# Optimization experiments

Measured on AMD Instinct MI355X. Metric: run time of the kernel, lower is better.

Reference implementation:

```python
import jax, jax.numpy as jnp
import numpy as np

# Structural constants (mirror init_kwargs)
P = 64    # n_poses
R = 128   # rotamers per pose
A = 8     # atoms per rotamer
EPS = 1e-2  # distance clamp to avoid singularity


def setup_inputs() -> dict:
    key = jax.random.key(0)
    n_rots = P * R
    coords = jax.random.normal(key, (n_rots * A, 3), dtype=jnp.float32) * 3.0
    coord_offset_for_rot = (jnp.arange(n_rots, dtype=jnp.int32) * A)
    pose_for_rot = jnp.repeat(jnp.arange(P, dtype=jnp.int32), R)
    rot_offset_for_pose = jnp.arange(P, dtype=jnp.int32) * R
    return {
        "coords": coords,
        "coord_offset_for_rot": coord_offset_for_rot,
        "pose_for_rot": pose_for_rot,
        "rot_offset_for_pose": rot_offset_for_pose,
    }


def reference(coords, coord_offset_for_rot, pose_for_rot, rot_offset_for_pose):
    # flatten leading dims to [n_atoms_total, 3] (matches coords.flatten(0,-2))
    flat = coords.reshape(-1, 3)
    # gather each rotamer's atoms via its coordinate offset: [n_rots, A]
    atom_idx = coord_offset_for_rot[:, None] + jnp.arange(A, dtype=jnp.int32)[None, :]
    x = flat[atom_idx]                       # [n_rots, A, 3]
    x = x.reshape(P, R, A, 3)                # block per pose
    # squared pairwise atom distances between all rotamer pairs within a pose
    sq = jnp.sum(x * x, axis=-1)             # [P, R, A]
    dot = jnp.einsum('piac,pjbc->pijab', x, x)   # [P, R, R, A, A]
    d2 = sq[:, :, None, :, None] + sq[:, None, :, None, :] - 2.0 * dot
    d2 = jnp.maximum(d2, EPS)
    # two subterm energies summed over atom pairs -> [P, R, R]
    s0 = jnp.sum(1.0 / d2, axis=(-2, -1))                  # LJ-like repulsion
    s1 = jnp.sum(jnp.exp(-jnp.sqrt(d2)), axis=(-2, -1))    # LK-like decay
    scores = jnp.stack([s0.reshape(-1), s1.reshape(-1)], axis=0)  # [2, nnz]
    # indices [3, nnz]: (pose, global rot_i, global rot_j)
    r = jnp.arange(R, dtype=jnp.int32)
    ii, jj = jnp.meshgrid(r, r, indexing='ij')             # [R, R]
    pose_idx = jnp.repeat(pose_for_rot, R)                 # [P*R*R]
    rot_i = (rot_offset_for_pose[:, None, None] + ii[None]).reshape(-1)
    rot_j = (rot_offset_for_pose[:, None, None] + jj[None]).reshape(-1)
    indices = jnp.stack([pose_idx, rot_i, rot_j], axis=0).astype(jnp.int32)
    return scores, indices
```

## Files before the change

### kernel.cpp

```cpp
#include <hip/hip_runtime.h>

typedef float v2f __attribute__((ext_vector_type(2)));

#define NPOSE 64
#define NROT  128
#define NATOM 8
#define EPS   1e-2f

#define TS    16
#define NTILE (NROT / TS)
#define NPAIR (NTILE * (NTILE + 1) / 2)
#define CSTR  28
#define SSTR  17

__global__ __launch_bounds__(256, 4) void rot_score_kernel(
    const float* __restrict__ coords,
    float* __restrict__ out)
{
    __shared__ float ldsI[TS * CSTR];
    __shared__ float ldsJ[TS * CSTR];
    __shared__ float res0[TS * SSTR];
    __shared__ float res1[TS * SSTR];

    const int bid = blockIdx.x;
    const int p   = bid / NPAIR;
    int t = bid - p * NPAIR;
    int ti = 0;
    while (t >= NTILE - ti) { t -= NTILE - ti; ++ti; }
    const int tj = ti + t;

    const int tid = threadIdx.x;
    const float* src = coords + (size_t)p * (NROT * NATOM * 3);

    for (int idx = tid; idx < 2 * TS * 24; idx += 256) {
        const int set = idx >= TS * 24;
        const int loc = idx - set * (TS * 24);
        const int r   = loc / 24;
        const int k   = loc - r * 24;
        const float v = src[(set ? tj : ti) * (TS * 24) + loc];
        (set ? ldsJ : ldsI)[r * CSTR + k] = v;
    }
    __syncthreads();

    const int ty = tid >> 4;
    const int tx = tid & 15;

    float4 xi4[6], xj4[6];
    {
        const float4* rowI = (const float4*)&ldsI[ty * CSTR];
        const float4* rowJ = (const float4*)&ldsJ[tx * CSTR];
#pragma unroll
        for (int k = 0; k < 6; ++k) { xi4[k] = rowI[k]; xj4[k] = rowJ[k]; }
    }
    float* xi = (float*)xi4;
    const float* xj = (const float*)xj4;

    float sqi[NATOM];
#pragma unroll
    for (int a = 0; a < NATOM; ++a)
        sqi[a] = fmaf(xi[a*3+2], xi[a*3+2], fmaf(xi[a*3+1], xi[a*3+1], xi[a*3+0]*xi[a*3+0]));
#pragma unroll
    for (int k = 0; k < 24; ++k) xi[k] = xi[k] * -2.0f;

    const float SCH_S = -12102203.0f;
    const float SCH_B = 1064866805.0f;
    const v2f veps = { EPS, EPS };

    v2f s0v = { 0.0f, 0.0f }, s1v = { 0.0f, 0.0f };

#pragma unroll
    for (int bp = 0; bp < 4; ++bp) {
        const v2f ax = { xj[bp*6 + 0], xj[bp*6 + 3] };
        const v2f ay = { xj[bp*6 + 1], xj[bp*6 + 4] };
        const v2f az = { xj[bp*6 + 2], xj[bp*6 + 5] };
        const v2f sj = __builtin_elementwise_fma(az, az,
                        __builtin_elementwise_fma(ay, ay, ax * ax));
#pragma unroll
        for (int a = 0; a < NATOM; ++a) {
            v2f t = sj + sqi[a];
            t = __builtin_elementwise_fma((v2f)(xi[a*3+0]), ax, t);
            t = __builtin_elementwise_fma((v2f)(xi[a*3+1]), ay, t);
            t = __builtin_elementwise_fma((v2f)(xi[a*3+2]), az, t);
            t = __builtin_elementwise_max(t, veps);
            const v2f rs = { __builtin_amdgcn_rsqf(t.x),
                             __builtin_amdgcn_rsqf(t.y) };
            s0v = __builtin_elementwise_fma(rs, rs, s0v);
            const v2f dv = t * rs;
            const v2f st = __builtin_elementwise_fma(dv, (v2f)(SCH_S), (v2f)(SCH_B));
            v2f e;
            e.x = __int_as_float((int)st.x);
            e.y = __int_as_float((int)st.y);
            s1v += e;
        }
    }
    const float s0 = s0v.x + s0v.y;
    const float s1 = s1v.x + s1v.y;

    res0[ty * SSTR + tx] = s0;
    res1[ty * SSTR + tx] = s1;

    const int nnz = NPOSE * NROT * NROT;
    const int gi  = ti * TS + ty;
    const int gj  = tj * TS + tx;
    const int n   = (p * NROT + gi) * NROT + gj;

    out[0 * nnz + n] = s0;
    out[1 * nnz + n] = s1;
    out[2 * nnz + n] = (float)p;
    out[3 * nnz + n] = (float)(p * NROT + gi);
    out[4 * nnz + n] = (float)(p * NROT + gj);

    if (ti != tj) {
        __syncthreads();
        const float m0 = res0[tx * SSTR + ty];
        const float m1 = res1[tx * SSTR + ty];
        const int mi = tj * TS + ty;
        const int mj = ti * TS + tx;
        const int nm = (p * NROT + mi) * NROT + mj;
        out[0 * nnz + nm] = m0;
        out[1 * nnz + nm] = m1;
        out[2 * nnz + nm] = (float)p;
        out[3 * nnz + nm] = (float)(p * NROT + mi);
        out[4 * nnz + nm] = (float)(p * NROT + mj);
    }
}

extern "C" void kernel_launch(void* const* d_in, const int* in_sizes, int n_in,
                              void* d_out, int out_size, void* d_ws, size_t ws_size,
                              hipStream_t stream) {
    (void)in_sizes; (void)n_in; (void)d_ws; (void)ws_size; (void)out_size;
    const float* coords = (const float*)d_in[0];
    float* out = (float*)d_out;

    dim3 grid(NPOSE * NPAIR);
    dim3 block(256);
    rot_score_kernel<<<grid, block, 0, stream>>>(coords, out);
}
```

Measured before the change: 19.06 us.

## Compute two j-rotamers per thread with 128-thread blocks and float2 stores

Halves the block to 128 threads and has each thread compute two output columns, packing the two j-rotamers into the v2f lanes instead of two atom pairs. The i-rotamer coordinates are reused across both columns, and all output writes become float2 vector stores. This cuts redundant loads of i-coordinates and the number of store instructions, but doubles per-thread work and register pressure and leaves fewer waves per block to hide latency.

```diff
diff --git a/kernel.cpp b/kernel.cpp
--- a/kernel.cpp
+++ b/kernel.cpp
@@ -13,7 +13,7 @@
 #define CSTR  28
 #define SSTR  17
 
-__global__ __launch_bounds__(256, 4) void rot_score_kernel(
+__global__ __launch_bounds__(128, 4) void rot_score_kernel(
     const float* __restrict__ coords,
     float* __restrict__ out)
 {
@@ -32,7 +32,7 @@
     const int tid = threadIdx.x;
     const float* src = coords + (size_t)p * (NROT * NATOM * 3);
 
-    for (int idx = tid; idx < 2 * TS * 24; idx += 256) {
+    for (int idx = tid; idx < 2 * TS * 24; idx += 128) {
         const int set = idx >= TS * 24;
         const int loc = idx - set * (TS * 24);
         const int r   = loc / 24;
@@ -42,18 +42,16 @@
     }
     __syncthreads();
 
-    const int ty = tid >> 4;
-    const int tx = tid & 15;
+    const int ty  = tid >> 3;
+    const int txp = tid & 7;
 
-    float4 xi4[6], xj4[6];
+    float4 xi4[6];
     {
         const float4* rowI = (const float4*)&ldsI[ty * CSTR];
-        const float4* rowJ = (const float4*)&ldsJ[tx * CSTR];
 #pragma unroll
-        for (int k = 0; k < 6; ++k) { xi4[k] = rowI[k]; xj4[k] = rowJ[k]; }
+        for (int k = 0; k < 6; ++k) xi4[k] = rowI[k];
     }
     float* xi = (float*)xi4;
-    const float* xj = (const float*)xj4;
 
     float sqi[NATOM];
 #pragma unroll
@@ -65,63 +63,88 @@
     const float SCH_S = -12102203.0f;
     const float SCH_B = 1064866805.0f;
     const v2f veps = { EPS, EPS };
+    const float* rowJA = &ldsJ[(txp * 2 + 0) * CSTR];
+    const float* rowJB = &ldsJ[(txp * 2 + 1) * CSTR];
 
     v2f s0v = { 0.0f, 0.0f }, s1v = { 0.0f, 0.0f };
 
 #pragma unroll
     for (int bp = 0; bp < 4; ++bp) {
-        const v2f ax = { xj[bp*6 + 0], xj[bp*6 + 3] };
-        const v2f ay = { xj[bp*6 + 1], xj[bp*6 + 4] };
-        const v2f az = { xj[bp*6 + 2], xj[bp*6 + 5] };
-        const v2f sj = __builtin_elementwise_fma(az, az,
-                        __builtin_elementwise_fma(ay, ay, ax * ax));
+        const float A0 = rowJA[bp*6 + 0], A1 = rowJA[bp*6 + 1], A2 = rowJA[bp*6 + 2];
+        const float A3 = rowJA[bp*6 + 3], A4 = rowJA[bp*6 + 4], A5 = rowJA[bp*6 + 5];
+        const float B0 = rowJB[bp*6 + 0], B1 = rowJB[bp*6 + 1], B2 = rowJB[bp*6 + 2];
+        const float B3 = rowJB[bp*6 + 3], B4 = rowJB[bp*6 + 4], B5 = rowJB[bp*6 + 5];
+        const v2f ex = { A0, B0 }, ey = { A1, B1 }, ez = { A2, B2 };
+        const v2f ox = { A3, B3 }, oy = { A4, B4 }, oz = { A5, B5 };
+        const v2f sje = __builtin_elementwise_fma(ez, ez,
+                         __builtin_elementwise_fma(ey, ey, ex * ex));
+        const v2f sjo = __builtin_elementwise_fma(oz, oz,
+                         __builtin_elementwise_fma(oy, oy, ox * ox));
 #pragma unroll
         for (int a = 0; a < NATOM; ++a) {
-            v2f t = sj + sqi[a];
-            t = __builtin_elementwise_fma((v2f)(xi[a*3+0]), ax, t);
-            t = __builtin_elementwise_fma((v2f)(xi[a*3+1]), ay, t);
-            t = __builtin_elementwise_fma((v2f)(xi[a*3+2]), az, t);
-            t = __builtin_elementwise_max(t, veps);
-            const v2f rs = { __builtin_amdgcn_rsqf(t.x),
-                             __builtin_amdgcn_rsqf(t.y) };
-            s0v = __builtin_elementwise_fma(rs, rs, s0v);
-            const v2f dv = t * rs;
-            const v2f st = __builtin_elementwise_fma(dv, (v2f)(SCH_S), (v2f)(SCH_B));
-            v2f e;
-            e.x = __int_as_float((int)st.x);
-            e.y = __int_as_float((int)st.y);
-            s1v += e;
+            v2f te = sje + sqi[a];
+            te = __builtin_elementwise_fma((v2f)(xi[a*3+0]), ex, te);
+            te = __builtin_elementwise_fma((v2f)(xi[a*3+1]), ey, te);
+            te = __builtin_elementwise_fma((v2f)(xi[a*3+2]), ez, te);
+            te = __builtin_elementwise_max(te, veps);
+            const v2f rse = { __builtin_amdgcn_rsqf(te.x), __builtin_amdgcn_rsqf(te.y) };
+            s0v = __builtin_elementwise_fma(rse, rse, s0v);
+            const v2f dve = te * rse;
+            const v2f ste = __builtin_elementwise_fma(dve, (v2f)(SCH_S), (v2f)(SCH_B));
+            v2f ee; ee.x = __int_as_float((int)ste.x); ee.y = __int_as_float((int)ste.y);
+            s1v += ee;
+
+            v2f to = sjo + sqi[a];
+            to = __builtin_elementwise_fma((v2f)(xi[a*3+0]), ox, to);
+            to = __builtin_elementwise_fma((v2f)(xi[a*3+1]), oy, to);
+            to = __builtin_elementwise_fma((v2f)(xi[a*3+2]), oz, to);
+            to = __builtin_elementwise_max(to, veps);
+            const v2f rso = { __builtin_amdgcn_rsqf(to.x), __builtin_amdgcn_rsqf(to.y) };
+            s0v = __builtin_elementwise_fma(rso, rso, s0v);
+            const v2f dvo = to * rso;
+            const v2f sto = __builtin_elementwise_fma(dvo, (v2f)(SCH_S), (v2f)(SCH_B));
+            v2f eo; eo.x = __int_as_float((int)sto.x); eo.y = __int_as_float((int)sto.y);
+            s1v += eo;
         }
     }
-    const float s0 = s0v.x + s0v.y;
-    const float s1 = s1v.x + s1v.y;
 
-    res0[ty * SSTR + tx] = s0;
-    res1[ty * SSTR + tx] = s1;
+    res0[ty * SSTR + txp * 2 + 0] = s0v.x;
+    res0[ty * SSTR + txp * 2 + 1] = s0v.y;
+    res1[ty * SSTR + txp * 2 + 0] = s1v.x;
+    res1[ty * SSTR + txp * 2 + 1] = s1v.y;
 
-    const int nnz = NPOSE * NROT * NROT;
-    const int gi  = ti * TS + ty;
-    const int gj  = tj * TS + tx;
-    const int n   = (p * NROT + gi) * NROT + gj;
+    const int nnz  = NPOSE * NROT * NROT;
+    const int gi   = ti * TS + ty;
+    const int col0 = tj * TS + txp * 2;
+    const int n    = (p * NROT + gi) * NROT + col0;
 
-    out[0 * nnz + n] = s0;
-    out[1 * nnz + n] = s1;
-    out[2 * nnz + n] = (float)p;
-    out[3 * nnz + n] = (float)(p * NROT + gi);
-    out[4 * nnz + n] = (float)(p * NROT + gj);
+    const float fp  = (float)p;
+    const float ri  = (float)(p * NROT + gi);
+    const float rj0 = (float)(p * NROT + col0);
+
+    *(float2*)(out + (size_t)0 * nnz + n) = make_float2(s0v.x, s0v.y);
+    *(float2*)(out + (size_t)1 * nnz + n) = make_float2(s1v.x, s1v.y);
+    *(float2*)(out + (size_t)2 * nnz + n) = make_float2(fp, fp);
+    *(float2*)(out + (size_t)3 * nnz + n) = make_float2(ri, ri);
+    *(float2*)(out + (size_t)4 * nnz + n) = make_float2(rj0, rj0 + 1.0f);
 
     if (ti != tj) {
         __syncthreads();
-        const float m0 = res0[tx * SSTR + ty];
-        const float m1 = res1[tx * SSTR + ty];
-        const int mi = tj * TS + ty;
-        const int mj = ti * TS + tx;
-        const int nm = (p * NROT + mi) * NROT + mj;
-        out[0 * nnz + nm] = m0;
-        out[1 * nnz + nm] = m1;
-        out[2 * nnz + nm] = (float)p;
-        out[3 * nnz + nm] = (float)(p * NROT + mi);
-        out[4 * nnz + nm] = (float)(p * NROT + mj);
+        const float m0a = res0[(txp * 2 + 0) * SSTR + ty];
+        const float m0b = res0[(txp * 2 + 1) * SSTR + ty];
+        const float m1a = res1[(txp * 2 + 0) * SSTR + ty];
+        const float m1b = res1[(txp * 2 + 1) * SSTR + ty];
+        const int mi    = tj * TS + ty;
+        const int mcol0 = ti * TS + txp * 2;
+        const int nm    = (p * NROT + mi) * NROT + mcol0;
+        const float mri  = (float)(p * NROT + mi);
+        const float mrj0 = (float)(p * NROT + mcol0);
+
+        *(float2*)(out + (size_t)0 * nnz + nm) = make_float2(m0a, m0b);
+        *(float2*)(out + (size_t)1 * nnz + nm) = make_float2(m1a, m1b);
+        *(float2*)(out + (size_t)2 * nnz + nm) = make_float2(fp, fp);
+        *(float2*)(out + (size_t)3 * nnz + nm) = make_float2(mri, mri);
+        *(float2*)(out + (size_t)4 * nnz + nm) = make_float2(mrj0, mrj0 + 1.0f);
     }
 }
 
@@ -133,6 +156,6 @@
     float* out = (float*)d_out;
 
     dim3 grid(NPOSE * NPAIR);
-    dim3 block(256);
+    dim3 block(128);
     rot_score_kernel<<<grid, block, 0, stream>>>(coords, out);
 }
```

New measurement: 20.61 us. 8.1% more time.
